# Optimization experiments

Hardware: AMD Instinct MI355X
Metric: run time of the kernel (lower is better)

## Reference

```python
import jax, jax.numpy as jnp
import numpy as np

M1, M2, BS = 2000, 400, 8
AT = M1 + M2
E1, E2, E3 = 60000, 20000, 20000
H, F, NG, L, C = 64, 64, 50, 4, 4
CUTOFF = 10.0
LOG2 = 0.6931471805599453  # shift of ShiftedSoftplus


def _ssp(x):
    return jax.nn.softplus(x) - LOG2


def _smear(d):
    # GaussianSmearing(0, cutoff, NG)
    offset = jnp.linspace(0.0, CUTOFF, NG)
    coeff = -0.5 / (offset[1] - offset[0]) ** 2
    return jnp.exp(coeff * (d[:, None] - offset[None, :]) ** 2)  # [E, NG]


def _colored_mlp(attr, colors, w1, b1, w2, b2):
    # w1:[C,NG,F] b1:[C,F] w2:[C,F,F] b2:[C,F]; route each edge through its color's MLP
    out = jnp.zeros((attr.shape[0], w1.shape[-1]), attr.dtype)
    for c in range(C):  # fixed small color count
        h = _ssp(attr @ w1[c] + b1[c]) @ w2[c] + b2[c]
        out = out + jnp.where((colors == c)[:, None], h, jnp.zeros((), attr.dtype))
    return out


def _block(h, ei, ew, attr, col, p):
    # InteractionBlock: CFConv -> ssp -> linear
    mw1, mb1, mw2, mb2, cw1, cw2, cb2, bw, bb = p
    Ccut = 0.5 * (jnp.cos(ew * jnp.pi / CUTOFF) + 1.0)
    W = _colored_mlp(attr, col, mw1, mb1, mw2, mb2) * Ccut[:, None]  # [E,F]
    x = h @ cw1                                   # lin1 (no bias) [N,F]
    msg = x[ei[:, 0]] * W                         # gather x_j, modulate
    agg = jax.ops.segment_sum(msg, ei[:, 1], num_segments=h.shape[0])  # scatter-add
    x = agg @ cw2 + cb2                           # lin2
    return _ssp(x) @ bw + bb                      # act + block linear


def _batch_graph(ei, ew, col):
    # replicate per-structure edges across the batch with node offset b*AT
    offs = (jnp.arange(BS, dtype=ei.dtype) * AT)[:, None, None]
    ei_b = (ei[None] + offs).reshape(-1, 2)
    return ei_b, jnp.tile(ew, BS), jnp.tile(col, BS)


def _forward(sites, sites_p, e1, ew1, c1, e2, ew2, c2, e3, ew3, c3,
             emb_w, emb_p_w, mlp_w1, mlp_b1, mlp_w2, mlp_b2,
             conv_w1, conv_w2, conv_b2, blk_w, blk_b,
             out_w1, out_b1, out_w2, out_b2):
    h = jnp.concatenate([emb_w[sites], emb_p_w[sites_p]], axis=1).reshape(BS * AT, H)
    graphs = []
    for (ei, ew, col) in ((e1, ew1, c1), (e2, ew2, c2), (e3, ew3, c3)):
        ei_b, ew_b, col_b = _batch_graph(ei, ew, col)
        graphs.append((ei_b, ew_b, col_b, _smear(ew_b)))
    for l in range(L):
        delta = jnp.zeros_like(h)
        for g, (ei_b, ew_b, col_b, attr_b) in enumerate(graphs):
            p = (mlp_w1[l, g], mlp_b1[l, g], mlp_w2[l, g], mlp_b2[l, g],
                 conv_w1[l, g], conv_w2[l, g], conv_b2[l, g], blk_w[l, g], blk_b[l, g])
            delta = delta + _block(h, ei_b, ew_b, attr_b, col_b, p)
        h = h + delta
    hp = h.reshape(BS, AT, H)[:, M1:, :]   # mask selects pore nodes only
    o = hp @ out_w1 + out_b1               # NB: original has `h - self.act(h)` no-op, so no activation here
    o = o @ out_w2 + out_b2                # [BS, M2, 1]
    return o.sum(axis=1)                   # 'add' readout per batch -> [BS, 1]


def setup_inputs() -> dict:
    key = jax.random.key(0)
    ks = jax.random.split(key, 24)
    f = lambda i, shape, s=0.1: jax.random.normal(ks[i], shape, jnp.float32) * s
    sites = jax.random.randint(ks[0], (BS, M1), 0, 1, dtype=jnp.int32)
    sites_p = jax.random.randint(ks[1], (BS, M2), 0, 2, dtype=jnp.int32)
    e1 = jax.random.randint(ks[2], (E1, 2), 0, M1, dtype=jnp.int32)
    e2 = jnp.stack([jax.random.randint(ks[3], (E2,), 0, M1, dtype=jnp.int32),
                    jax.random.randint(ks[4], (E2,), M1, AT, dtype=jnp.int32)], 1)
    e3 = jnp.stack([jax.random.randint(ks[5], (E3,), M1, AT, dtype=jnp.int32),
                    jax.random.randint(ks[6], (E3,), 0, M1, dtype=jnp.int32)], 1)
    ew1 = jax.random.uniform(ks[7], (E1,), jnp.float32, 0.5, CUTOFF)
    ew2 = jax.random.uniform(ks[8], (E2,), jnp.float32, 0.5, CUTOFF)
    ew3 = jax.random.uniform(ks[9], (E3,), jnp.float32, 0.5, CUTOFF)
    c1 = jax.random.randint(ks[10], (E1,), 0, C, dtype=jnp.int32)
    c2 = jax.random.randint(ks[11], (E2,), 0, C, dtype=jnp.int32)
    c3 = jax.random.randint(ks[12], (E3,), 0, C, dtype=jnp.int32)
    return {
        'sites': sites, 'sites_p': sites_p,
        'edge_idx1': e1, 'edge_weight1': ew1, 'colors1': c1,
        'edge_idx2': e2, 'edge_weight2': ew2, 'colors2': c2,
        'edge_idx3': e3, 'edge_weight3': ew3, 'colors3': c3,
        'emb_w': f(13, (1, H), 1.0), 'emb_p_w': f(14, (2, H), 1.0),
        'mlp_w1': f(15, (L, 3, C, NG, F)), 'mlp_b1': jnp.zeros((L, 3, C, F), jnp.float32),
        'mlp_w2': f(16, (L, 3, C, F, F)), 'mlp_b2': jnp.zeros((L, 3, C, F), jnp.float32),
        'conv_w1': f(17, (L, 3, H, F)), 'conv_w2': f(18, (L, 3, F, H)),
        'conv_b2': jnp.zeros((L, 3, H), jnp.float32),
        'blk_w': f(19, (L, 3, H, H)), 'blk_b': jnp.zeros((L, 3, H), jnp.float32),
        'out_w1': f(20, (H, H // 2)), 'out_b1': jnp.zeros((H // 2,), jnp.float32),
        'out_w2': f(21, (H // 2, 1)), 'out_b2': jnp.zeros((1,), jnp.float32),
    }


def reference(sites, sites_p, edge_idx1, edge_weight1, colors1,
              edge_idx2, edge_weight2, colors2, edge_idx3, edge_weight3, colors3,
              emb_w, emb_p_w, mlp_w1, mlp_b1, mlp_w2, mlp_b2,
              conv_w1, conv_w2, conv_b2, blk_w, blk_b,
              out_w1, out_b1, out_w2, out_b2):
    return _forward(sites, sites_p, edge_idx1, edge_weight1, colors1,
                    edge_idx2, edge_weight2, colors2, edge_idx3, edge_weight3, colors3,
                    emb_w, emb_p_w, mlp_w1, mlp_b1, mlp_w2, mlp_b2,
                    conv_w1, conv_w2, conv_b2, blk_w, blk_b,
                    out_w1, out_b1, out_w2, out_b2)
```

## Files before the change

kernel.cpp:

```cpp
#include <hip/hip_runtime.h>
#include <math.h>

constexpr int M1 = 2000, M2 = 400, BS = 8;
constexpr int AT = M1 + M2;
constexpr int NN = BS * AT;
constexpr int E1 = 60000, E2 = 20000, E3 = 20000;
constexpr int ET = E1 + E2 + E3;
constexpr int H = 64, F = 64, NG = 50, L = 4, C = 4;
constexpr float CUTOFF = 10.0f;
constexpr float LOG2F_ = 0.6931471805599453f;

constexpr float SMEAR_STEP = 10.0f / 49.0f;
constexpr float SMEAR_COEFF = -12.005f;
constexpr float PI_OVER_CUT = 0.31415926535897932f;

constexpr int NBLK = (ET + 255) / 256;

constexpr int NT = 256;
constexpr float DSCALE = (float)(NT - 1) / CUTOFF;

constexpr int TILE_M = 32;
constexpr int MT = NN / TILE_M;

constexpr int NB0 = M1 / 4;
constexpr int NB1 = M2 / 4;
constexpr int NB2 = M1 / 4;
constexpr int NBTOT = NB0 + NB1 + NB2;

constexpr int LT0 = M1 / 4;
constexpr int LT1 = M1 / 4;
constexpr int LT2 = M2 / 4;
constexpr int LTOT = LT0 + LT1 + LT2;

constexpr int A_TAB  = 48 * NT / 4;
constexpr int A_INIT = NN * 64 / 256;
constexpr int A_CNT  = NBLK;
constexpr int A_CV   = 3;
constexpr int A_TOT  = A_TAB + A_INIT + A_CNT + A_CV;
constexpr int B_PACK = 48 * NT * 64 / 256;
constexpr int B_TOT  = B_PACK + 3 + 3;

constexpr size_t O_HA    = 0;
constexpr size_t O_HB    = O_HA  + (size_t)NN * 64 * 4;
constexpr size_t O_XG    = O_HB  + (size_t)NN * 64 * 4;
constexpr size_t O_DG    = O_XG  + (size_t)3 * AT * 512 * 2;
constexpr size_t O_TAB2  = O_DG  + (size_t)3 * NN * 64 * 4;
constexpr size_t O_EDATA = O_TAB2 + (size_t)48 * NT * 64 * 4;
constexpr size_t O_INT   = O_EDATA + (size_t)ET * 16;
constexpr int I_DEG  = 0;
constexpr int I_CUR  = 7200;
constexpr int I_ZEND = 14400;
constexpr int I_BASE = 14400;
constexpr int I_PERM = 21616;
constexpr int I_CV   = 26016;

__device__ inline float sspf(float x) {
    return fmaxf(x, 0.0f) + log1pf(expf(-fabsf(x))) - LOG2F_;
}
__device__ inline float sspf_fast(float x) {
    float t = __expf(-fabsf(x));
    return fmaxf(x, 0.0f) + __logf(1.0f + t) - LOG2F_;
}

__device__ inline unsigned int bf16rn(float x) {
    unsigned int u = __float_as_uint(x);
    u = (u + 0x7FFFu + ((u >> 16) & 1u)) >> 16;
    return u & 0xFFFFu;
}

__device__ inline int graph_off(int g) { return g == 0 ? 0 : (g == 1 ? E1 : E1 + E2); }

__device__ inline void edge_decode(int idx, int& g, int& e,
                                   const int* ei1, const int* ei2, const int* ei3,
                                   const int* c1, const int* c2, const int* c3,
                                   const int*& ei, const int*& cl) {
    if (idx < E1)            { g = 0; e = idx;           ei = ei1; cl = c1; }
    else if (idx < E1 + E2)  { g = 1; e = idx - E1;      ei = ei2; cl = c2; }
    else                     { g = 2; e = idx - E1 - E2; ei = ei3; cl = c3; }
}

__global__ __launch_bounds__(256) void k_setupA(
    const float* __restrict__ mlp_w1, const float* __restrict__ mlp_b1,
    const float* __restrict__ mlp_w2, const float* __restrict__ mlp_b2,
    float* __restrict__ tabF,
    const int* __restrict__ sites, const int* __restrict__ sites_p,
    const float* __restrict__ emb_w, const float* __restrict__ emb_p_w,
    float* __restrict__ h,
    const int* __restrict__ ei1, const int* __restrict__ ei2,
    const int* __restrict__ ei3, const int* __restrict__ c1,
    const int* __restrict__ c2, const int* __restrict__ c3,
    int* __restrict__ deg,
    const float* __restrict__ conv_b2, const float* __restrict__ blk_w,
    const float* __restrict__ blk_b, float* __restrict__ cvbuf) {
    int bid = blockIdx.x;
    int t = threadIdx.x;
    if (bid < A_TAB) {
        const int lane = t & 63;
        int w = bid * 4 + (t >> 6);
        int s = w / NT;
        int p = w - s * NT;
        int l = s % L;
        int gc = s / L;
        int c = gc % C;
        int g = gc / C;
        float d = (float)p * (CUTOFF / (float)(NT - 1));
        size_t wb = (size_t)((l * 3 + g) * C + c);
        const float* w1 = mlp_w1 + wb * NG * F;
        const float* w2 = mlp_w2 + wb * F * F;
        float w1c[NG], w2c[F];
        #pragma unroll
        for (int k = 0; k < NG; k++) w1c[k] = w1[k * F + lane];
        #pragma unroll
        for (int k = 0; k < F; k++) w2c[k] = w2[k * F + lane];
        float b1c = mlp_b1[wb * F + lane];
        float b2c = mlp_b2[wb * F + lane];
        float dd = d - (float)lane * SMEAR_STEP;
        float av = (lane < NG) ? __expf(SMEAR_COEFF * dd * dd) : 0.0f;
        float acc = b1c;
        #pragma unroll
        for (int k = 0; k < NG; k++) acc = fmaf(__shfl(av, k), w1c[k], acc);
        float tt = sspf_fast(acc);
        float acc2 = b2c;
        #pragma unroll
        for (int j = 0; j < F; j++) acc2 = fmaf(__shfl(tt, j), w2c[j], acc2);
        float ccut = 0.5f * (__cosf(d * PI_OVER_CUT) + 1.0f);
        tabF[((size_t)s * NT + p) * 64 + lane] = acc2 * ccut;
    } else if (bid < A_TAB + A_INIT) {
        int idx = (bid - A_TAB) * 256 + t;
        int f = idx & 63;
        int n = idx >> 6;
        int b = n / AT;
        int i = n - b * AT;
        float v;
        if (i < M1) v = emb_w[sites[b * M1 + i] * H + f];
        else        v = emb_p_w[sites_p[b * M2 + (i - M1)] * H + f];
        h[idx] = v;
    } else if (bid < A_TAB + A_INIT + A_CNT) {
        int idx = (bid - A_TAB - A_INIT) * 256 + t;
        if (idx < ET) {
            int g, e; const int* ei; const int* cl;
            edge_decode(idx, g, e, ei1, ei2, ei3, c1, c2, c3, ei, cl);
            atomicAdd(&deg[g * AT + ei[2 * e + 1]], 1);
        }
    } else {
        int s = (bid - A_TAB - A_INIT - A_CNT) * 4 + (t >> 6);
        int lane = t & 63;
        if (s < 12) {
            float sl = sspf(conv_b2[s * 64 + lane]);
            const float* bw = blk_w + (size_t)s * 4096;
            float a = blk_b[s * 64 + lane];
            #pragma unroll 8
            for (int k = 0; k < 64; k++)
                a = fmaf(__shfl(sl, k), bw[k * 64 + lane], a);
            cvbuf[s * 64 + lane] = a;
        }
    }
}

__global__ __launch_bounds__(256) void k_setupB(
    const float* __restrict__ tabF, unsigned int* __restrict__ tab2,
    const int* __restrict__ deg, int* __restrict__ base,
    int* __restrict__ perm) {
    int bid = blockIdx.x;
    int t = threadIdx.x;
    if (bid < B_PACK) {
        int idx = bid * 256 + t;
        int pc = idx & (NT * 64 - 1);
        int nxt = (pc < (NT - 1) * 64) ? idx + 64 : idx;
        unsigned int lo = bf16rn(tabF[idx]);
        unsigned int hi = bf16rn(tabF[nxt]);
        tab2[idx] = lo | (hi << 16);
    } else if (bid < B_PACK + 3) {
        const int T = 256, CH = 10;
        __shared__ int lsum[256];
        int g = bid - B_PACK;
        int loc[CH];
        int s = 0;
        #pragma unroll
        for (int i = 0; i < CH; i++) {
            int idx = t * CH + i;
            int v = (idx < AT) ? deg[g * AT + idx] : 0;
            loc[i] = s;
            s += v;
        }
        lsum[t] = s;
        __syncthreads();
        for (int off = 1; off < T; off <<= 1) {
            int v = 0;
            if (t >= off) v = lsum[t - off];
            __syncthreads();
            lsum[t] += v;
            __syncthreads();
        }
        int tb = lsum[t] - s;
        #pragma unroll
        for (int i = 0; i < CH; i++) {
            int idx = t * CH + i;
            if (idx < AT) base[g * (AT + 1) + idx] = tb + loc[i];
        }
        if (t == T - 1) base[g * (AT + 1) + AT] = lsum[T - 1];
    } else {
        __shared__ int hist[256];
        __shared__ int cur[256];
        int g = bid - B_PACK - 3;
        int off   = (g == 1) ? M1 : 0;
        int cnt   = (g == 1) ? M2 : M1;
        int pbase = (g == 0) ? 0 : ((g == 1) ? M1 : (M1 + M2));
        hist[t] = 0;
        __syncthreads();
        for (int i = t; i < cnt; i += 256)
            atomicAdd(&hist[min(deg[g * AT + off + i], 255)], 1);
        __syncthreads();
        if (t == 0) {
            int run = 0;
            for (int k = 0; k < 256; k++) { cur[k] = run; run += hist[k]; }
        }
        __syncthreads();
        for (int i = t; i < cnt; i += 256) {
            int pos = atomicAdd(&cur[min(deg[g * AT + off + i], 255)], 1);
            perm[pbase + pos] = off + i;
        }
    }
}

__global__ void k_fill(const int* __restrict__ ei1, const int* __restrict__ ei2,
                       const int* __restrict__ ei3, const int* __restrict__ c1,
                       const int* __restrict__ c2, const int* __restrict__ c3,
                       const float* __restrict__ ew1, const float* __restrict__ ew2,
                       const float* __restrict__ ew3,
                       const int* __restrict__ base, int* __restrict__ cur,
                       int4* __restrict__ edata) {
    int idx = blockIdx.x * blockDim.x + threadIdx.x;
    if (idx >= ET) return;
    int g, e; const int* ei; const int* cl;
    edge_decode(idx, g, e, ei1, ei2, ei3, c1, c2, c3, ei, cl);
    const float* ew = (g == 0) ? ew1 : (g == 1 ? ew2 : ew3);
    int dst = ei[2 * e + 1];
    int src = ei[2 * e];
    int p = base[g * (AT + 1) + dst] + atomicAdd(&cur[g * AT + dst], 1);
    float t = ew[e] * DSCALE;
    int i0 = min((int)t, NT - 2);
    float fr = t - (float)i0;
    int cb = cl[e] * (L * NT) + i0;
    edata[graph_off(g) + p] = make_int4(src, cb, __float_as_int(fr), 0);
}

__device__ inline void fma4(float acc[4], float a, const float4 b) {
    acc[0] = fmaf(a, b.x, acc[0]);
    acc[1] = fmaf(a, b.y, acc[1]);
    acc[2] = fmaf(a, b.z, acc[2]);
    acc[3] = fmaf(a, b.w, acc[3]);
}

__device__ inline void stage_B(const float* __restrict__ gB, float (*Bs)[68], int t) {
    #pragma unroll
    for (int i = 0; i < 4; i++) {
        int v = t + i * 256;
        int r = v >> 4, c4 = (v & 15) * 4;
        *(float4*)&Bs[r][c4] = *(const float4*)(gB + (size_t)r * 64 + c4);
    }
}
__device__ inline void gemm_tile(const float (*As)[68], const float (*Bs)[68],
                                 int r0, int c0, float acc0[4], float acc1[4]) {
    #pragma unroll 4
    for (int k0 = 0; k0 < 64; k0 += 4) {
        float4 a0 = *(const float4*)&As[r0][k0];
        float4 a1 = *(const float4*)&As[r0 + 1][k0];
        float4 b0 = *(const float4*)&Bs[k0][c0];
        float4 b1 = *(const float4*)&Bs[k0 + 1][c0];
        float4 b2 = *(const float4*)&Bs[k0 + 2][c0];
        float4 b3 = *(const float4*)&Bs[k0 + 3][c0];
        fma4(acc0, a0.x, b0); fma4(acc0, a0.y, b1);
        fma4(acc0, a0.z, b2); fma4(acc0, a0.w, b3);
        fma4(acc1, a1.x, b0); fma4(acc1, a1.y, b1);
        fma4(acc1, a1.z, b2); fma4(acc1, a1.w, b3);
    }
}

__device__ inline void xg_transpose_store(const float (*T)[68],
                                          unsigned short* __restrict__ xg,
                                          int g, int i0, int t) {
    int k = t >> 6, c = t & 63;
    unsigned int w0 = bf16rn(T[k * 8 + 0][c]) | (bf16rn(T[k * 8 + 1][c]) << 16);
    unsigned int w1 = bf16rn(T[k * 8 + 2][c]) | (bf16rn(T[k * 8 + 3][c]) << 16);
    unsigned int w2 = bf16rn(T[k * 8 + 4][c]) | (bf16rn(T[k * 8 + 5][c]) << 16);
    unsigned int w3 = bf16rn(T[k * 8 + 6][c]) | (bf16rn(T[k * 8 + 7][c]) << 16);
    unsigned short* out = xg + (((size_t)g * AT + i0 + k) * 64 + c) * 8;
    *(uint4*)out = make_uint4(w0, w1, w2, w3);
}

__device__ inline void lin1_map(int bid, int& g, int& igrp) {
    if (bid < LT0)            { g = 0; igrp = bid; }
    else if (bid < LT0 + LT1) { g = 1; igrp = bid - LT0; }
    else                      { g = 2; igrp = LT0 + (bid - LT0 - LT1); }
}

__global__ __launch_bounds__(256) void k_lin1t(
    const float* __restrict__ h, const float* __restrict__ conv_w1,
    unsigned short* __restrict__ xg, int l) {
    __shared__ float As[TILE_M][68];
    __shared__ float Bs[64][68];
    int t = threadIdx.x;
    int g, igrp;
    lin1_map(blockIdx.x, g, igrp);
    int i0 = igrp * 4;
    #pragma unroll
    for (int it = 0; it < 2; it++) {
        int v = t + it * 256;
        int r = v >> 4, c4 = (v & 15) * 4;
        int n = (r & 7) * AT + i0 + (r >> 3);
        *(float4*)&As[r][c4] = *(const float4*)(h + (size_t)n * 64 + c4);
    }
    stage_B(conv_w1 + (size_t)(l * 3 + g) * 4096, Bs, t);
    __syncthreads();
    int cg = t & 15, rg = t >> 4;
    int c0 = cg * 4, r0 = rg * 2;
    float acc0[4] = {0, 0, 0, 0}, acc1[4] = {0, 0, 0, 0};
    gemm_tile(As, Bs, r0, c0, acc0, acc1);
    __syncthreads();
    *(float4*)&As[r0][c0]     = make_float4(acc0[0], acc0[1], acc0[2], acc0[3]);
    *(float4*)&As[r0 + 1][c0] = make_float4(acc1[0], acc1[1], acc1[2], acc1[3]);
    __syncthreads();
    xg_transpose_store(As, xg, g, i0, t);
}

__global__ __launch_bounds__(256) void k_aggl(
    const int4* __restrict__ edata, const int* __restrict__ base,
    const int* __restrict__ perm,
    const unsigned short* __restrict__ xg, const unsigned int* __restrict__ tab2,
    const float* __restrict__ conv_w2, const float* __restrict__ conv_b2,
    const float* __restrict__ blk_w, const float* __restrict__ blk_b,
    float* __restrict__ dg, int l) {
    __shared__ float As[TILE_M][68];
    __shared__ float Bs[64][68];
    int t = threadIdx.x;
    const int lane = t & 63;
    const int wv = t >> 6;
    int bid = blockIdx.x;
    int g, grp, nbg, pbase;
    if (bid < NB0)            { g = 0; grp = bid;             nbg = NB0; pbase = 0; }
    else if (bid < NB0 + NB1) { g = 1; grp = bid - NB0;       nbg = NB1; pbase = M1; }
    else                      { g = 2; grp = bid - NB0 - NB1; nbg = NB2; pbase = M1 + M2; }
    int gi = nbg - 1 - grp;
    int dst = perm[pbase + gi * 4 + wv];
    size_t pb = (size_t)(l * 3 + g);
    stage_B(conv_w2 + pb * 4096, Bs, t);

    const int4* ed = edata + graph_off(g);
    int s = base[g * (AT + 1) + dst];
    int e = base[g * (AT + 1) + dst + 1];
    const unsigned int* tg = tab2 + ((size_t)g * C * L * NT + (size_t)l * NT) * 64;
    const unsigned short* xgg = xg + (size_t)g * AT * 512;
    float acc[8];
    #pragma unroll
    for (int j = 0; j < 8; j++) acc[j] = 0.0f;

    int i = s;
    while (i < e) {
        int cnt = min(e - i, 64);
        int4 mrec = ed[i + min(lane, cnt - 1)];
        int j = 0;
        for (; j + 2 <= cnt; j += 2) {
            int x0 = __shfl(mrec.x, j),     y0 = __shfl(mrec.y, j),     z0 = __shfl(mrec.z, j);
            int x1 = __shfl(mrec.x, j + 1), y1 = __shfl(mrec.y, j + 1), z1 = __shfl(mrec.z, j + 1);
            unsigned int u0 = tg[(size_t)y0 * 64 + lane];
            unsigned int u1 = tg[(size_t)y1 * 64 + lane];
            uint4 q0 = *(const uint4*)(xgg + ((size_t)x0 * 64 + lane) * 8);
            uint4 q1 = *(const uint4*)(xgg + ((size_t)x1 * 64 + lane) * 8);
            float lo0 = __uint_as_float(u0 << 16);
            float hi0 = __uint_as_float(u0 & 0xFFFF0000u);
            float lo1 = __uint_as_float(u1 << 16);
            float hi1 = __uint_as_float(u1 & 0xFFFF0000u);
            float wl0 = fmaf(__int_as_float(z0), hi0 - lo0, lo0);
            float wl1 = fmaf(__int_as_float(z1), hi1 - lo1, lo1);
            acc[0] = fmaf(__uint_as_float(q0.x << 16),         wl0, acc[0]);
            acc[1] = fmaf(__uint_as_float(q0.x & 0xFFFF0000u), wl0, acc[1]);
            acc[2] = fmaf(__uint_as_float(q0.y << 16),         wl0, acc[2]);
            acc[3] = fmaf(__uint_as_float(q0.y & 0xFFFF0000u), wl0, acc[3]);
            acc[4] = fmaf(__uint_as_float(q0.z << 16),         wl0, acc[4]);
            acc[5] = fmaf(__uint_as_float(q0.z & 0xFFFF0000u), wl0, acc[5]);
            acc[6] = fmaf(__uint_as_float(q0.w << 16),         wl0, acc[6]);
            acc[7] = fmaf(__uint_as_float(q0.w & 0xFFFF0000u), wl0, acc[7]);
            acc[0] = fmaf(__uint_as_float(q1.x << 16),         wl1, acc[0]);
            acc[1] = fmaf(__uint_as_float(q1.x & 0xFFFF0000u), wl1, acc[1]);
            acc[2] = fmaf(__uint_as_float(q1.y << 16),         wl1, acc[2]);
            acc[3] = fmaf(__uint_as_float(q1.y & 0xFFFF0000u), wl1, acc[3]);
            acc[4] = fmaf(__uint_as_float(q1.z << 16),         wl1, acc[4]);
            acc[5] = fmaf(__uint_as_float(q1.z & 0xFFFF0000u), wl1, acc[5]);
            acc[6] = fmaf(__uint_as_float(q1.w << 16),         wl1, acc[6]);
            acc[7] = fmaf(__uint_as_float(q1.w & 0xFFFF0000u), wl1, acc[7]);
        }
        if (j < cnt) {
            int x0 = __shfl(mrec.x, j), y0 = __shfl(mrec.y, j), z0 = __shfl(mrec.z, j);
            unsigned int u0 = tg[(size_t)y0 * 64 + lane];
            uint4 q = *(const uint4*)(xgg + ((size_t)x0 * 64 + lane) * 8);
            float lo0 = __uint_as_float(u0 << 16);
            float hi0 = __uint_as_float(u0 & 0xFFFF0000u);
            float wl = fmaf(__int_as_float(z0), hi0 - lo0, lo0);
            acc[0] = fmaf(__uint_as_float(q.x << 16),         wl, acc[0]);
            acc[1] = fmaf(__uint_as_float(q.x & 0xFFFF0000u), wl, acc[1]);
            acc[2] = fmaf(__uint_as_float(q.y << 16),         wl, acc[2]);
            acc[3] = fmaf(__uint_as_float(q.y & 0xFFFF0000u), wl, acc[3]);
            acc[4] = fmaf(__uint_as_float(q.z << 16),         wl, acc[4]);
            acc[5] = fmaf(__uint_as_float(q.z & 0xFFFF0000u), wl, acc[5]);
            acc[6] = fmaf(__uint_as_float(q.w << 16),         wl, acc[6]);
            acc[7] = fmaf(__uint_as_float(q.w & 0xFFFF0000u), wl, acc[7]);
        }
        i += cnt;
    }
    #pragma unroll
    for (int b2 = 0; b2 < 8; b2++) As[wv * 8 + b2][lane] = acc[b2];
    __syncthreads();

    int cg = t & 15, rg = t >> 4;
    int cc0 = cg * 4, r0 = rg * 2;
    float4 bias = *(const float4*)(conv_b2 + pb * 64 + cc0);
    float a0[4] = {bias.x, bias.y, bias.z, bias.w};
    float a1[4] = {bias.x, bias.y, bias.z, bias.w};
    gemm_tile(As, Bs, r0, cc0, a0, a1);
    __syncthreads();
    *(float4*)&As[r0][cc0] =
        make_float4(sspf(a0[0]), sspf(a0[1]), sspf(a0[2]), sspf(a0[3]));
    *(float4*)&As[r0 + 1][cc0] =
        make_float4(sspf(a1[0]), sspf(a1[1]), sspf(a1[2]), sspf(a1[3]));
    stage_B(blk_w + pb * 4096, Bs, t);
    __syncthreads();
    float4 bb = *(const float4*)(blk_b + pb * 64 + cc0);
    float b0[4] = {bb.x, bb.y, bb.z, bb.w};
    float b1[4] = {bb.x, bb.y, bb.z, bb.w};
    gemm_tile(As, Bs, r0, cc0, b0, b1);
    int dstR = perm[pbase + gi * 4 + (r0 >> 3)];
    float* dp0 = dg + ((size_t)g * NN + (size_t)(r0 & 7) * AT + dstR) * 64 + cc0;
    float* dp1 = dg + ((size_t)g * NN + (size_t)((r0 + 1) & 7) * AT + dstR) * 64 + cc0;
    *(float4*)dp0 = make_float4(b0[0], b0[1], b0[2], b0[3]);
    *(float4*)dp1 = make_float4(b1[0], b1[1], b1[2], b1[3]);
}

__global__ __launch_bounds__(256) void k_lin1f(
    const float* __restrict__ hIn, float* __restrict__ hOut,
    const float* __restrict__ dg, const float* __restrict__ conv_w1,
    const float* __restrict__ cvbuf,
    unsigned short* __restrict__ xg, int lcur, int last) {
    __shared__ float As[TILE_M][68];
    __shared__ float Bs[64][68];
    int t = threadIdx.x;
    int g, igrp;
    if (last) { g = 0; igrp = blockIdx.x; }
    else      lin1_map(blockIdx.x, g, igrp);
    int i0 = igrp * 4;
    int writeH = last ? 1 : (g != 1);
    const float* cvl = cvbuf + (size_t)lcur * 3 * 64;
    #pragma unroll
    for (int it = 0; it < 2; it++) {
        int v = t + it * 256;
        int r = v >> 4, c4 = (v & 15) * 4;
        int k = r >> 3, b = r & 7;
        int node_i = i0 + k;
        size_t o = ((size_t)b * AT + node_i) * 64 + c4;
        float4 hv = *(const float4*)(hIn + o);
        if (node_i < M1) {
            float4 d0 = *(const float4*)(dg + o);
            float4 d2 = *(const float4*)(dg + (size_t)2 * NN * 64 + o);
            float4 c1v = *(const float4*)(cvl + 64 + c4);
            hv.x += d0.x + c1v.x + d2.x;
            hv.y += d0.y + c1v.y + d2.y;
            hv.z += d0.z + c1v.z + d2.z;
            hv.w += d0.w + c1v.w + d2.w;
        } else {
            float4 d1 = *(const float4*)(dg + (size_t)NN * 64 + o);
            float4 c0v = *(const float4*)(cvl + c4);
            float4 c2v = *(const float4*)(cvl + 128 + c4);
            hv.x += c0v.x + d1.x + c2v.x;
            hv.y += c0v.y + d1.y + c2v.y;
            hv.z += c0v.z + d1.z + c2v.z;
            hv.w += c0v.w + d1.w + c2v.w;
        }
        *(float4*)&As[r][c4] = hv;
        if (writeH) *(float4*)(hOut + o) = hv;
    }
    if (last) return;
    stage_B(conv_w1 + (size_t)((lcur + 1) * 3 + g) * 4096, Bs, t);
    __syncthreads();
    int cg = t & 15, rg = t >> 4;
    int c0 = cg * 4, r0 = rg * 2;
    float acc0[4] = {0, 0, 0, 0}, acc1[4] = {0, 0, 0, 0};
    gemm_tile(As, Bs, r0, c0, acc0, acc1);
    __syncthreads();
    *(float4*)&As[r0][c0]     = make_float4(acc0[0], acc0[1], acc0[2], acc0[3]);
    *(float4*)&As[r0 + 1][c0] = make_float4(acc1[0], acc1[1], acc1[2], acc1[3]);
    __syncthreads();
    xg_transpose_store(As, xg, g, i0, t);
}

__global__ void k_read(const float* __restrict__ h,
                       const float* __restrict__ w1, const float* __restrict__ b1,
                       const float* __restrict__ w2, const float* __restrict__ b2,
                       float* __restrict__ out) {
    int b = blockIdx.x;
    int lane = threadIdx.x & 63;
    int wv = threadIdx.x >> 6;
    __shared__ float part[4];
    float weff = 0.0f;
    #pragma unroll
    for (int j = 0; j < H / 2; j++) weff = fmaf(w1[lane * (H / 2) + j], w2[j], weff);
    float acc = 0.0f;
    for (int i = wv * (M2 / 4); i < (wv + 1) * (M2 / 4); i++)
        acc += h[((size_t)b * AT + M1 + i) * H + lane];
    float v = acc * weff;
    for (int off = 32; off; off >>= 1) v += __shfl_xor(v, off);
    if (lane == 0) part[wv] = v;
    __syncthreads();
    if (threadIdx.x == 0) {
        float bias = b2[0];
        for (int j = 0; j < H / 2; j++) bias = fmaf(b1[j], w2[j], bias);
        out[b] = part[0] + part[1] + part[2] + part[3] + (float)M2 * bias;
    }
}

extern "C" void kernel_launch(void* const* d_in, const int* in_sizes, int n_in,
                              void* d_out, int out_size, void* d_ws, size_t ws_size,
                              hipStream_t stream) {
    const int* sites   = (const int*)d_in[0];
    const int* sites_p = (const int*)d_in[1];
    const int* ei1 = (const int*)d_in[2];
    const float* ew1 = (const float*)d_in[3];
    const int* c1 = (const int*)d_in[4];
    const int* ei2 = (const int*)d_in[5];
    const float* ew2 = (const float*)d_in[6];
    const int* c2 = (const int*)d_in[7];
    const int* ei3 = (const int*)d_in[8];
    const float* ew3 = (const float*)d_in[9];
    const int* c3 = (const int*)d_in[10];
    const float* emb_w   = (const float*)d_in[11];
    const float* emb_p_w = (const float*)d_in[12];
    const float* mlp_w1 = (const float*)d_in[13];
    const float* mlp_b1 = (const float*)d_in[14];
    const float* mlp_w2 = (const float*)d_in[15];
    const float* mlp_b2 = (const float*)d_in[16];
    const float* conv_w1 = (const float*)d_in[17];
    const float* conv_w2 = (const float*)d_in[18];
    const float* conv_b2 = (const float*)d_in[19];
    const float* blk_w = (const float*)d_in[20];
    const float* blk_b = (const float*)d_in[21];
    const float* out_w1 = (const float*)d_in[22];
    const float* out_b1 = (const float*)d_in[23];
    const float* out_w2 = (const float*)d_in[24];
    const float* out_b2 = (const float*)d_in[25];

    char* ws = (char*)d_ws;
    float* hA   = (float*)(ws + O_HA);
    float* hB   = (float*)(ws + O_HB);
    unsigned short* xg = (unsigned short*)(ws + O_XG);
    float* dg   = (float*)(ws + O_DG);
    unsigned int* tab2 = (unsigned int*)(ws + O_TAB2);
    int4*  edata = (int4*)(ws + O_EDATA);
    int* ip    = (int*)(ws + O_INT);
    int* deg   = ip + I_DEG;
    int* cur   = ip + I_CUR;
    int* ibase = ip + I_BASE;
    int* dperm = ip + I_PERM;
    float* cvbuf = (float*)(ip + I_CV);

    hipMemsetAsync(ip, 0, (size_t)I_ZEND * sizeof(int), stream);

    k_setupA<<<A_TOT, 256, 0, stream>>>(mlp_w1, mlp_b1, mlp_w2, mlp_b2, dg,
                                        sites, sites_p, emb_w, emb_p_w, hA,
                                        ei1, ei2, ei3, c1, c2, c3, deg,
                                        conv_b2, blk_w, blk_b, cvbuf);
    k_setupB<<<B_TOT, 256, 0, stream>>>(dg, tab2, deg, ibase, dperm);
    k_fill<<<NBLK, 256, 0, stream>>>(ei1, ei2, ei3, c1, c2, c3, ew1, ew2, ew3,
                                     ibase, cur, edata);

    k_lin1t<<<LTOT, 256, 0, stream>>>(hA, conv_w1, xg, 0);
    float* hcur = hA;
    float* hnxt = hB;
    for (int l = 0; l < L; l++) {
        int last = (l == L - 1) ? 1 : 0;
        k_aggl<<<NBTOT, 256, 0, stream>>>(edata, ibase, dperm, xg, tab2,
                                          conv_w2, conv_b2, blk_w, blk_b,
                                          dg, l);
        k_lin1f<<<last ? MT : LTOT, 256, 0, stream>>>(hcur, hnxt, dg, conv_w1,
                                                      cvbuf, xg, l, last);
        float* tmp = hcur; hcur = hnxt; hnxt = tmp;
    }
    k_read<<<BS, 256, 0, stream>>>(hcur, out_w1, out_b1, out_w2, out_b2, (float*)d_out);
}
```

Before: 325.3 us.

## Fuse per-layer aggregation, residual update and next lin1 into one kernel

Merges the aggregation kernel and the residual/lin1 kernel into a single per-layer kernel that owns destination nodes. Site tiles gather both graph 0 and graph 2 messages, and pore tiles gather graph 1. Each tile applies lin2, ssp and the block linear, adds the residual and constant terms, then computes the next layer's lin1 projections directly. This removes the dg intermediate round trip and one launch per layer, and the degree sort now keys site nodes on their combined degree. The cost is fewer, heavier blocks (600 instead of 1100) with imbalanced work between site and pore tiles, which may reduce parallelism.

```diff
diff --git a/kernel.cpp b/kernel.cpp
--- a/kernel.cpp
+++ b/kernel.cpp
@@ -20,12 +20,10 @@
 constexpr float DSCALE = (float)(NT - 1) / CUTOFF;
 
 constexpr int TILE_M = 32;
-constexpr int MT = NN / TILE_M;
-
-constexpr int NB0 = M1 / 4;
-constexpr int NB1 = M2 / 4;
-constexpr int NB2 = M1 / 4;
-constexpr int NBTOT = NB0 + NB1 + NB2;
+
+constexpr int SITE_T = M1 / 4;
+constexpr int PORE_T = M2 / 4;
+constexpr int NTILE  = SITE_T + PORE_T;
 
 constexpr int LT0 = M1 / 4;
 constexpr int LT1 = M1 / 4;
@@ -38,7 +36,7 @@
 constexpr int A_CV   = 3;
 constexpr int A_TOT  = A_TAB + A_INIT + A_CNT + A_CV;
 constexpr int B_PACK = 48 * NT * 64 / 256;
-constexpr int B_TOT  = B_PACK + 3 + 3;
+constexpr int B_TOT  = B_PACK + 3 + 2;
 
 constexpr size_t O_HA    = 0;
 constexpr size_t O_HB    = O_HA  + (size_t)NN * 64 * 4;
@@ -202,14 +200,15 @@
     } else {
         __shared__ int hist[256];
         __shared__ int cur[256];
-        int g = bid - B_PACK - 3;
-        int off   = (g == 1) ? M1 : 0;
-        int cnt   = (g == 1) ? M2 : M1;
-        int pbase = (g == 0) ? 0 : ((g == 1) ? M1 : (M1 + M2));
+        int q = bid - B_PACK - 3;
+        int cnt   = q ? M2 : M1;
+        int obase = q ? M1 : 0;
         hist[t] = 0;
         __syncthreads();
-        for (int i = t; i < cnt; i += 256)
-            atomicAdd(&hist[min(deg[g * AT + off + i], 255)], 1);
+        for (int i = t; i < cnt; i += 256) {
+            int key = q ? deg[AT + M1 + i] : (deg[i] + deg[2 * AT + i]);
+            atomicAdd(&hist[min(key, 255)], 1);
+        }
         __syncthreads();
         if (t == 0) {
             int run = 0;
@@ -217,8 +216,9 @@
         }
         __syncthreads();
         for (int i = t; i < cnt; i += 256) {
-            int pos = atomicAdd(&cur[min(deg[g * AT + off + i], 255)], 1);
-            perm[pbase + pos] = off + i;
+            int key = q ? deg[AT + M1 + i] : (deg[i] + deg[2 * AT + i]);
+            int pos = atomicAdd(&cur[min(key, 255)], 1);
+            perm[obase + pos] = q ? (M1 + i) : i;
         }
     }
 }
@@ -289,6 +289,20 @@
     *(uint4*)out = make_uint4(w0, w1, w2, w3);
 }
 
+__device__ inline void xg_tstore(const float (*T)[68],
+                                 unsigned short* __restrict__ xg,
+                                 int g, const int* __restrict__ perm,
+                                 int pbase, int gi, int t) {
+    int k = t >> 6, c = t & 63;
+    int node = perm[pbase + gi * 4 + k];
+    unsigned int w0 = bf16rn(T[k * 8 + 0][c]) | (bf16rn(T[k * 8 + 1][c]) << 16);
+    unsigned int w1 = bf16rn(T[k * 8 + 2][c]) | (bf16rn(T[k * 8 + 3][c]) << 16);
+    unsigned int w2 = bf16rn(T[k * 8 + 4][c]) | (bf16rn(T[k * 8 + 5][c]) << 16);
+    unsigned int w3 = bf16rn(T[k * 8 + 6][c]) | (bf16rn(T[k * 8 + 7][c]) << 16);
+    unsigned short* out = xg + (((size_t)g * AT + node) * 64 + c) * 8;
+    *(uint4*)out = make_uint4(w0, w1, w2, w3);
+}
+
 __device__ inline void lin1_map(int bid, int& g, int& igrp) {
     if (bid < LT0)            { g = 0; igrp = bid; }
     else if (bid < LT0 + LT1) { g = 1; igrp = bid - LT0; }
@@ -324,37 +338,10 @@
     xg_transpose_store(As, xg, g, i0, t);
 }
 
-__global__ __launch_bounds__(256) void k_aggl(
-    const int4* __restrict__ edata, const int* __restrict__ base,
-    const int* __restrict__ perm,
-    const unsigned short* __restrict__ xg, const unsigned int* __restrict__ tab2,
-    const float* __restrict__ conv_w2, const float* __restrict__ conv_b2,
-    const float* __restrict__ blk_w, const float* __restrict__ blk_b,
-    float* __restrict__ dg, int l) {
-    __shared__ float As[TILE_M][68];
-    __shared__ float Bs[64][68];
-    int t = threadIdx.x;
-    const int lane = t & 63;
-    const int wv = t >> 6;
-    int bid = blockIdx.x;
-    int g, grp, nbg, pbase;
-    if (bid < NB0)            { g = 0; grp = bid;             nbg = NB0; pbase = 0; }
-    else if (bid < NB0 + NB1) { g = 1; grp = bid - NB0;       nbg = NB1; pbase = M1; }
-    else                      { g = 2; grp = bid - NB0 - NB1; nbg = NB2; pbase = M1 + M2; }
-    int gi = nbg - 1 - grp;
-    int dst = perm[pbase + gi * 4 + wv];
-    size_t pb = (size_t)(l * 3 + g);
-    stage_B(conv_w2 + pb * 4096, Bs, t);
-
-    const int4* ed = edata + graph_off(g);
-    int s = base[g * (AT + 1) + dst];
-    int e = base[g * (AT + 1) + dst + 1];
-    const unsigned int* tg = tab2 + ((size_t)g * C * L * NT + (size_t)l * NT) * 64;
-    const unsigned short* xgg = xg + (size_t)g * AT * 512;
-    float acc[8];
-    #pragma unroll
-    for (int j = 0; j < 8; j++) acc[j] = 0.0f;
-
+__device__ inline void gather_dst(const int4* __restrict__ ed, int s, int e,
+                                  const unsigned int* __restrict__ tg,
+                                  const unsigned short* __restrict__ xgg,
+                                  int lane, float acc[8]) {
     int i = s;
     while (i < e) {
         int cnt = min(e - i, 64);
@@ -408,88 +395,143 @@
         }
         i += cnt;
     }
-    #pragma unroll
-    for (int b2 = 0; b2 < 8; b2++) As[wv * 8 + b2][lane] = acc[b2];
-    __syncthreads();
-
-    int cg = t & 15, rg = t >> 4;
-    int cc0 = cg * 4, r0 = rg * 2;
-    float4 bias = *(const float4*)(conv_b2 + pb * 64 + cc0);
-    float a0[4] = {bias.x, bias.y, bias.z, bias.w};
-    float a1[4] = {bias.x, bias.y, bias.z, bias.w};
-    gemm_tile(As, Bs, r0, cc0, a0, a1);
-    __syncthreads();
-    *(float4*)&As[r0][cc0] =
-        make_float4(sspf(a0[0]), sspf(a0[1]), sspf(a0[2]), sspf(a0[3]));
-    *(float4*)&As[r0 + 1][cc0] =
-        make_float4(sspf(a1[0]), sspf(a1[1]), sspf(a1[2]), sspf(a1[3]));
-    stage_B(blk_w + pb * 4096, Bs, t);
-    __syncthreads();
-    float4 bb = *(const float4*)(blk_b + pb * 64 + cc0);
-    float b0[4] = {bb.x, bb.y, bb.z, bb.w};
-    float b1[4] = {bb.x, bb.y, bb.z, bb.w};
-    gemm_tile(As, Bs, r0, cc0, b0, b1);
-    int dstR = perm[pbase + gi * 4 + (r0 >> 3)];
-    float* dp0 = dg + ((size_t)g * NN + (size_t)(r0 & 7) * AT + dstR) * 64 + cc0;
-    float* dp1 = dg + ((size_t)g * NN + (size_t)((r0 + 1) & 7) * AT + dstR) * 64 + cc0;
-    *(float4*)dp0 = make_float4(b0[0], b0[1], b0[2], b0[3]);
-    *(float4*)dp1 = make_float4(b1[0], b1[1], b1[2], b1[3]);
-}
-
-__global__ __launch_bounds__(256) void k_lin1f(
+}
+
+__global__ __launch_bounds__(256) void k_layer(
+    const int4* __restrict__ edata, const int* __restrict__ base,
+    const int* __restrict__ perm,
+    unsigned short* __restrict__ xg, const unsigned int* __restrict__ tab2,
+    const float* __restrict__ conv_w2, const float* __restrict__ conv_b2,
+    const float* __restrict__ blk_w, const float* __restrict__ blk_b,
+    const float* __restrict__ conv_w1, const float* __restrict__ cvbuf,
     const float* __restrict__ hIn, float* __restrict__ hOut,
-    const float* __restrict__ dg, const float* __restrict__ conv_w1,
-    const float* __restrict__ cvbuf,
-    unsigned short* __restrict__ xg, int lcur, int last) {
+    int l, int last) {
     __shared__ float As[TILE_M][68];
     __shared__ float Bs[64][68];
     int t = threadIdx.x;
-    int g, igrp;
-    if (last) { g = 0; igrp = blockIdx.x; }
-    else      lin1_map(blockIdx.x, g, igrp);
-    int i0 = igrp * 4;
-    int writeH = last ? 1 : (g != 1);
-    const float* cvl = cvbuf + (size_t)lcur * 3 * 64;
+    const int lane = t & 63;
+    const int wv = t >> 6;
+    int bid = blockIdx.x;
+    int site = (bid < SITE_T) ? 1 : 0;
+    int gi = site ? (SITE_T - 1 - bid) : (PORE_T - 1 - (bid - SITE_T));
+    int pbperm = site ? 0 : M1;
+    int gA = site ? 0 : 1;
+    int dst = perm[pbperm + gi * 4 + wv];
+    size_t pbA = (size_t)(l * 3 + gA);
+    stage_B(conv_w2 + pbA * 4096, Bs, t);
+
+    float accA[8], accB[8];
     #pragma unroll
-    for (int it = 0; it < 2; it++) {
-        int v = t + it * 256;
-        int r = v >> 4, c4 = (v & 15) * 4;
-        int k = r >> 3, b = r & 7;
-        int node_i = i0 + k;
-        size_t o = ((size_t)b * AT + node_i) * 64 + c4;
-        float4 hv = *(const float4*)(hIn + o);
-        if (node_i < M1) {
-            float4 d0 = *(const float4*)(dg + o);
-            float4 d2 = *(const float4*)(dg + (size_t)2 * NN * 64 + o);
-            float4 c1v = *(const float4*)(cvl + 64 + c4);
-            hv.x += d0.x + c1v.x + d2.x;
-            hv.y += d0.y + c1v.y + d2.y;
-            hv.z += d0.z + c1v.z + d2.z;
-            hv.w += d0.w + c1v.w + d2.w;
-        } else {
-            float4 d1 = *(const float4*)(dg + (size_t)NN * 64 + o);
-            float4 c0v = *(const float4*)(cvl + c4);
-            float4 c2v = *(const float4*)(cvl + 128 + c4);
-            hv.x += c0v.x + d1.x + c2v.x;
-            hv.y += c0v.y + d1.y + c2v.y;
-            hv.z += c0v.z + d1.z + c2v.z;
-            hv.w += c0v.w + d1.w + c2v.w;
-        }
-        *(float4*)&As[r][c4] = hv;
-        if (writeH) *(float4*)(hOut + o) = hv;
-    }
-    if (last) return;
-    stage_B(conv_w1 + (size_t)((lcur + 1) * 3 + g) * 4096, Bs, t);
-    __syncthreads();
+    for (int j = 0; j < 8; j++) { accA[j] = 0.0f; accB[j] = 0.0f; }
+    {
+        int s = base[gA * (AT + 1) + dst];
+        int e = base[gA * (AT + 1) + dst + 1];
+        gather_dst(edata + graph_off(gA), s, e,
+                   tab2 + ((size_t)gA * C * L + l) * NT * 64,
+                   xg + (size_t)gA * AT * 512, lane, accA);
+    }
+    if (site) {
+        int s = base[2 * (AT + 1) + dst];
+        int e = base[2 * (AT + 1) + dst + 1];
+        gather_dst(edata + graph_off(2), s, e,
+                   tab2 + ((size_t)2 * C * L + l) * NT * 64,
+                   xg + (size_t)2 * AT * 512, lane, accB);
+    }
+    #pragma unroll
+    for (int b = 0; b < 8; b++) As[wv * 8 + b][lane] = accA[b];
+    __syncthreads();
+
     int cg = t & 15, rg = t >> 4;
     int c0 = cg * 4, r0 = rg * 2;
-    float acc0[4] = {0, 0, 0, 0}, acc1[4] = {0, 0, 0, 0};
-    gemm_tile(As, Bs, r0, c0, acc0, acc1);
-    __syncthreads();
-    *(float4*)&As[r0][c0]     = make_float4(acc0[0], acc0[1], acc0[2], acc0[3]);
-    *(float4*)&As[r0 + 1][c0] = make_float4(acc1[0], acc1[1], acc1[2], acc1[3]);
-    __syncthreads();
-    xg_transpose_store(As, xg, g, i0, t);
+    float4 cbA = *(const float4*)(conv_b2 + pbA * 64 + c0);
+    float x0[4] = {cbA.x, cbA.y, cbA.z, cbA.w};
+    float x1[4] = {cbA.x, cbA.y, cbA.z, cbA.w};
+    gemm_tile(As, Bs, r0, c0, x0, x1);
+    __syncthreads();
+    *(float4*)&As[r0][c0] =
+        make_float4(sspf(x0[0]), sspf(x0[1]), sspf(x0[2]), sspf(x0[3]));
+    *(float4*)&As[r0 + 1][c0] =
+        make_float4(sspf(x1[0]), sspf(x1[1]), sspf(x1[2]), sspf(x1[3]));
+    stage_B(blk_w + pbA * 4096, Bs, t);
+    __syncthreads();
+
+    int kk = r0 >> 3, b0 = r0 & 7;
+    int nodek = perm[pbperm + gi * 4 + kk];
+    size_t o0 = ((size_t)b0 * AT + nodek) * 64 + c0;
+    size_t o1 = o0 + (size_t)AT * 64;
+    float4 h0 = *(const float4*)(hIn + o0);
+    float4 h1 = *(const float4*)(hIn + o1);
+    const float* cvl = cvbuf + (size_t)l * 3 * 64;
+    float4 bbA = *(const float4*)(blk_b + pbA * 64 + c0);
+    float4 ex;
+    if (site) {
+        float4 bbB = *(const float4*)(blk_b + (size_t)(l * 3 + 2) * 64 + c0);
+        float4 c1v = *(const float4*)(cvl + 64 + c0);
+        ex = make_float4(bbB.x + c1v.x, bbB.y + c1v.y, bbB.z + c1v.z, bbB.w + c1v.w);
+    } else {
+        float4 c0v = *(const float4*)(cvl + c0);
+        float4 c2v = *(const float4*)(cvl + 128 + c0);
+        ex = make_float4(c0v.x + c2v.x, c0v.y + c2v.y, c0v.z + c2v.z, c0v.w + c2v.w);
+    }
+    float d0[4] = {h0.x + bbA.x + ex.x, h0.y + bbA.y + ex.y,
+                   h0.z + bbA.z + ex.z, h0.w + bbA.w + ex.w};
+    float d1[4] = {h1.x + bbA.x + ex.x, h1.y + bbA.y + ex.y,
+                   h1.z + bbA.z + ex.z, h1.w + bbA.w + ex.w};
+    gemm_tile(As, Bs, r0, c0, d0, d1);
+
+    if (site) {
+        __syncthreads();
+        #pragma unroll
+        for (int b = 0; b < 8; b++) As[wv * 8 + b][lane] = accB[b];
+        stage_B(conv_w2 + (size_t)(l * 3 + 2) * 4096, Bs, t);
+        __syncthreads();
+        float4 cbB = *(const float4*)(conv_b2 + (size_t)(l * 3 + 2) * 64 + c0);
+        float y0[4] = {cbB.x, cbB.y, cbB.z, cbB.w};
+        float y1[4] = {cbB.x, cbB.y, cbB.z, cbB.w};
+        gemm_tile(As, Bs, r0, c0, y0, y1);
+        __syncthreads();
+        *(float4*)&As[r0][c0] =
+            make_float4(sspf(y0[0]), sspf(y0[1]), sspf(y0[2]), sspf(y0[3]));
+        *(float4*)&As[r0 + 1][c0] =
+            make_float4(sspf(y1[0]), sspf(y1[1]), sspf(y1[2]), sspf(y1[3]));
+        stage_B(blk_w + (size_t)(l * 3 + 2) * 4096, Bs, t);
+        __syncthreads();
+        gemm_tile(As, Bs, r0, c0, d0, d1);
+    }
+
+    *(float4*)(hOut + o0) = make_float4(d0[0], d0[1], d0[2], d0[3]);
+    *(float4*)(hOut + o1) = make_float4(d1[0], d1[1], d1[2], d1[3]);
+    if (last) return;
+
+    __syncthreads();
+    *(float4*)&As[r0][c0]     = make_float4(d0[0], d0[1], d0[2], d0[3]);
+    *(float4*)&As[r0 + 1][c0] = make_float4(d1[0], d1[1], d1[2], d1[3]);
+    int gB = site ? 0 : 2;
+    stage_B(conv_w1 + (size_t)((l + 1) * 3 + gB) * 4096, Bs, t);
+    __syncthreads();
+    float p0[4] = {0, 0, 0, 0}, p1[4] = {0, 0, 0, 0};
+    gemm_tile(As, Bs, r0, c0, p0, p1);
+    if (site) {
+        __syncthreads();
+        stage_B(conv_w1 + (size_t)((l + 1) * 3 + 1) * 4096, Bs, t);
+        __syncthreads();
+        float q0[4] = {0, 0, 0, 0}, q1[4] = {0, 0, 0, 0};
+        gemm_tile(As, Bs, r0, c0, q0, q1);
+        __syncthreads();
+        *(float4*)&As[r0][c0]     = make_float4(p0[0], p0[1], p0[2], p0[3]);
+        *(float4*)&As[r0 + 1][c0] = make_float4(p1[0], p1[1], p1[2], p1[3]);
+        *(float4*)&Bs[r0][c0]     = make_float4(q0[0], q0[1], q0[2], q0[3]);
+        *(float4*)&Bs[r0 + 1][c0] = make_float4(q1[0], q1[1], q1[2], q1[3]);
+        __syncthreads();
+        xg_tstore(As, xg, 0, perm, pbperm, gi, t);
+        xg_tstore((const float(*)[68])Bs, xg, 1, perm, pbperm, gi, t);
+    } else {
+        __syncthreads();
+        *(float4*)&As[r0][c0]     = make_float4(p0[0], p0[1], p0[2], p0[3]);
+        *(float4*)&As[r0 + 1][c0] = make_float4(p1[0], p1[1], p1[2], p1[3]);
+        __syncthreads();
+        xg_tstore(As, xg, 2, perm, pbperm, gi, t);
+    }
 }
 
 __global__ void k_read(const float* __restrict__ h,
@@ -551,7 +593,7 @@
     float* hA   = (float*)(ws + O_HA);
     float* hB   = (float*)(ws + O_HB);
     unsigned short* xg = (unsigned short*)(ws + O_XG);
-    float* dg   = (float*)(ws + O_DG);
+    float* tabF = (float*)(ws + O_DG);
     unsigned int* tab2 = (unsigned int*)(ws + O_TAB2);
     int4*  edata = (int4*)(ws + O_EDATA);
     int* ip    = (int*)(ws + O_INT);
@@ -563,11 +605,11 @@
 
     hipMemsetAsync(ip, 0, (size_t)I_ZEND * sizeof(int), stream);
 
-    k_setupA<<<A_TOT, 256, 0, stream>>>(mlp_w1, mlp_b1, mlp_w2, mlp_b2, dg,
+    k_setupA<<<A_TOT, 256, 0, stream>>>(mlp_w1, mlp_b1, mlp_w2, mlp_b2, tabF,
                                         sites, sites_p, emb_w, emb_p_w, hA,
                                         ei1, ei2, ei3, c1, c2, c3, deg,
                                         conv_b2, blk_w, blk_b, cvbuf);
-    k_setupB<<<B_TOT, 256, 0, stream>>>(dg, tab2, deg, ibase, dperm);
+    k_setupB<<<B_TOT, 256, 0, stream>>>(tabF, tab2, deg, ibase, dperm);
     k_fill<<<NBLK, 256, 0, stream>>>(ei1, ei2, ei3, c1, c2, c3, ew1, ew2, ew3,
                                      ibase, cur, edata);
 
@@ -576,11 +618,9 @@
     float* hnxt = hB;
     for (int l = 0; l < L; l++) {
         int last = (l == L - 1) ? 1 : 0;
-        k_aggl<<<NBTOT, 256, 0, stream>>>(edata, ibase, dperm, xg, tab2,
-                                          conv_w2, conv_b2, blk_w, blk_b,
-                                          dg, l);
-        k_lin1f<<<last ? MT : LTOT, 256, 0, stream>>>(hcur, hnxt, dg, conv_w1,
-                                                      cvbuf, xg, l, last);
+        k_layer<<<NTILE, 256, 0, stream>>>(edata, ibase, dperm, xg, tab2,
+                                           conv_w2, conv_b2, blk_w, blk_b,
+                                           conv_w1, cvbuf, hcur, hnxt, l, last);
         float* tmp = hcur; hcur = hnxt; hnxt = tmp;
     }
     k_read<<<BS, 256, 0, stream>>>(hcur, out_w1, out_b1, out_w2, out_b2, (float*)d_out);
```

Result: no change. 323.1 us (-0.7%).
